# Kernel optimization log

Hardware: AMD Instinct MI355X
Metric: run time of the kernel (lower is better)

## Reference

```python
import jax, jax.numpy as jnp
import numpy as np

WS = 8          # window size
N = WS * WS     # tokens per window (64)
C = 256         # embed dim
H = 8           # heads
D = C // H      # head dim (32)
NW = 256        # windows per image
B_ = 2048       # total windows in batch (8 images * 256 windows)
CPB_HIDDEN = 512


def _make_relative_position_index():
    coords_h = np.arange(WS)
    coords_w = np.arange(WS)
    coords = np.stack(np.meshgrid(coords_h, coords_w, indexing='ij'))  # [2,WS,WS]
    coords = coords.reshape(2, -1)                                     # [2,N]
    rel = coords[:, :, None] - coords[:, None, :]                      # [2,N,N]
    rel = rel.transpose(1, 2, 0).astype(np.int64)                      # [N,N,2]
    rel[:, :, 0] += WS - 1
    rel[:, :, 1] += WS - 1
    rel[:, :, 0] *= 2 * WS - 1
    return rel.sum(-1)                                                 # [N,N]


def _make_relative_coords_table():
    rh = np.arange(-(WS - 1), WS, dtype=np.float64)
    rw = np.arange(-(WS - 1), WS, dtype=np.float64)
    tbl = np.stack(np.meshgrid(rh, rw, indexing='ij')).transpose(1, 2, 0)[None]  # [1,2W-1,2W-1,2]
    tbl[:, :, :, 0] /= (WS - 1)  # pretrained_window_size == window_size
    tbl[:, :, :, 1] /= (WS - 1)
    tbl *= 8
    tbl = np.sign(tbl) * np.log2(np.abs(tbl) + 1.0) / np.log2(8)
    return tbl.astype(np.float32)


def setup_inputs() -> dict:
    key = jax.random.key(0)
    ks = jax.random.split(key, 8)
    x = jax.random.normal(ks[0], (B_, N, C), dtype=jnp.float32)
    # shifted-window style additive mask: 0 for allowed, -100 for masked
    mask_bits = jax.random.uniform(ks[1], (NW, N, N)) < 0.1
    mask = jnp.where(mask_bits, jnp.float32(-100.0), jnp.float32(0.0))
    qkv_w = jax.random.normal(ks[2], (C, 3 * C), dtype=jnp.float32) * (1.0 / np.sqrt(C))
    q_bias = jnp.zeros((C,), jnp.float32)
    v_bias = jnp.zeros((C,), jnp.float32)
    logit_scale = jnp.full((H, 1, 1), np.log(10.0), dtype=jnp.float32)
    coords_table = jnp.asarray(_make_relative_coords_table())
    mlp1_w = jax.random.normal(ks[3], (2, CPB_HIDDEN), dtype=jnp.float32) * 0.5
    mlp1_b = jnp.zeros((CPB_HIDDEN,), jnp.float32)
    mlp2_w = jax.random.normal(ks[4], (CPB_HIDDEN, H), dtype=jnp.float32) * (1.0 / np.sqrt(CPB_HIDDEN))
    proj_w = jax.random.normal(ks[5], (C, C), dtype=jnp.float32) * (1.0 / np.sqrt(C))
    proj_b = jnp.zeros((C,), jnp.float32)
    rel_pos_index = jnp.asarray(_make_relative_position_index())  # [N,N] int64
    return {
        'x': x, 'mask': mask, 'qkv_w': qkv_w, 'q_bias': q_bias, 'v_bias': v_bias,
        'logit_scale': logit_scale, 'coords_table': coords_table,
        'mlp1_w': mlp1_w, 'mlp1_b': mlp1_b, 'mlp2_w': mlp2_w,
        'proj_w': proj_w, 'proj_b': proj_b, 'rel_pos_index': rel_pos_index,
    }


def _l2norm(t, axis=-1, eps=1e-12):
    n = jnp.sqrt(jnp.sum(t * t, axis=axis, keepdims=True))
    return t / jnp.maximum(n, eps)


def reference(x, mask, qkv_w, q_bias, v_bias, logit_scale, coords_table,
              mlp1_w, mlp1_b, mlp2_w, proj_w, proj_b, rel_pos_index):
    b, n, c = x.shape
    # qkv projection with (q_bias, 0, v_bias)
    qkv_bias = jnp.concatenate([q_bias, jnp.zeros_like(v_bias), v_bias], axis=0)
    qkv = x @ qkv_w + qkv_bias                          # [b, n, 3c]
    qkv = qkv.reshape(b, n, 3, H, D).transpose(2, 0, 3, 1, 4)  # [3, b, H, n, D]
    q, k, v = qkv[0], qkv[1], qkv[2]
    # cosine attention with learned per-head logit scale
    attn = jnp.einsum('bhnd,bhmd->bhnm', _l2norm(q), _l2norm(k))
    scale = jnp.exp(jnp.minimum(logit_scale, jnp.float32(np.log(1.0 / 0.01))))  # [H,1,1]
    attn = attn * scale[None]                           # [b, H, n, n]
    # continuous position bias MLP
    hbt = jax.nn.relu(coords_table @ mlp1_w + mlp1_b)   # [1, 2W-1, 2W-1, 512]
    bias_table = (hbt @ mlp2_w).reshape(-1, H)          # [(2W-1)^2, H]
    rel_bias = bias_table[rel_pos_index.reshape(-1)].reshape(n, n, H)
    rel_bias = 16.0 * jax.nn.sigmoid(rel_bias.transpose(2, 0, 1))  # [H, n, n]
    attn = attn + rel_bias[None]
    # shifted-window mask
    nw = mask.shape[0]
    attn = attn.reshape(b // nw, nw, H, n, n) + mask[None, :, None]
    attn = attn.reshape(b, H, n, n)
    attn = jax.nn.softmax(attn, axis=-1)
    out = jnp.einsum('bhnm,bhmd->bnhd', attn, v).reshape(b, n, c)
    return out @ proj_w + proj_b
```

## Files before the change

kernel.cpp:

```cpp
#include <hip/hip_runtime.h>
#include <hip/hip_bf16.h>
#include <stdint.h>

#define NTOK   64
#define CDIM   256
#define NHEAD  8
#define DHEAD  32
#define NWIN   256
#define BWIN   2048
#define MROWS  131072

typedef __attribute__((ext_vector_type(8))) short short8;
typedef __attribute__((ext_vector_type(4))) float f32x4;

__device__ __forceinline__ ushort f2bf(float f) {
  uint32_t u = __float_as_uint(f);
  u += 0x7fffu + ((u >> 16) & 1u);
  return (ushort)(u >> 16);
}
__device__ __forceinline__ void unpack8(uint4 u, float* f) {
  f[0] = __uint_as_float(u.x << 16);
  f[1] = __uint_as_float(u.x & 0xffff0000u);
  f[2] = __uint_as_float(u.y << 16);
  f[3] = __uint_as_float(u.y & 0xffff0000u);
  f[4] = __uint_as_float(u.z << 16);
  f[5] = __uint_as_float(u.z & 0xffff0000u);
  f[6] = __uint_as_float(u.w << 16);
  f[7] = __uint_as_float(u.w & 0xffff0000u);
}


__global__ void k_cast_bf16(const float* __restrict__ src, ushort* __restrict__ dst, int n4) {
  int i = blockIdx.x * blockDim.x + threadIdx.x;
  int stride = gridDim.x * blockDim.x;
  for (; i < n4; i += stride) {
    float4 v = ((const float4*)src)[i];
    ushort4 o;
    o.x = f2bf(v.x); o.y = f2bf(v.y); o.z = f2bf(v.z); o.w = f2bf(v.w);
    ((ushort4*)dst)[i] = o;
  }
}

__global__ void k_transpose_bf16(const float* __restrict__ src, ushort* __restrict__ dst, int K, int N) {
  int idx = blockIdx.x * 256 + threadIdx.x;
  if (idx < N * K) {
    int n = idx / K, k = idx - n * K;
    dst[idx] = f2bf(src[(size_t)k * N + n]);
  }
}

__global__ void k_cpb(const float* __restrict__ ct, const float* __restrict__ w1,
                      const float* __restrict__ b1, const float* __restrict__ w2,
                      float* __restrict__ out) {
  int p = blockIdx.x, t = threadIdx.x;
  float c0 = ct[p * 2], c1 = ct[p * 2 + 1];
  float acc[8];
#pragma unroll
  for (int h = 0; h < 8; ++h) acc[h] = 0.f;
  for (int j = t; j < 512; j += 256) {
    float hj = fmaxf(0.f, fmaf(c0, w1[j], fmaf(c1, w1[512 + j], b1[j])));
#pragma unroll
    for (int h = 0; h < 8; ++h) acc[h] = fmaf(hj, w2[j * 8 + h], acc[h]);
  }
#pragma unroll
  for (int off = 1; off < 64; off <<= 1)
#pragma unroll
    for (int h = 0; h < 8; ++h) acc[h] += __shfl_xor(acc[h], off, 64);
  __shared__ float red[4][8];
  if ((t & 63) == 0)
#pragma unroll
    for (int h = 0; h < 8; ++h) red[t >> 6][h] = acc[h];
  __syncthreads();
  if (t < 8) out[p * 8 + t] = red[0][t] + red[1][t] + red[2][t] + red[3][t];
}

__global__ void k_relbC(const float* __restrict__ bt, const int* __restrict__ rpi,
                        float* __restrict__ out) {
  int idx = blockIdx.x * 256 + threadIdx.x;
  int reg = idx & 3, l16 = (idx >> 2) & 15, g = (idx >> 6) & 3;
  int nt = (idx >> 8) & 3, mt = (idx >> 10) & 3, h = idx >> 12;
  int r = mt * 16 + g * 4 + reg, c = nt * 16 + l16;
  float v = bt[rpi[r * 64 + c] * 8 + h];
  out[idx] = 16.0f / (1.0f + __expf(-v));
}

__global__ void k_maskC(const float* __restrict__ mask, float* __restrict__ out) {
  int idx = blockIdx.x * 256 + threadIdx.x;
  int reg = idx & 3, l16 = (idx >> 2) & 15, g = (idx >> 6) & 3;
  int nt = (idx >> 8) & 3, mt = (idx >> 10) & 3, wi = idx >> 12;
  int r = mt * 16 + g * 4 + reg, c = nt * 16 + l16;
  out[idx] = mask[(size_t)wi * 4096 + r * 64 + c];
}

template <int MODE>
__global__ __launch_bounds__(256, 2) void gemm_bt(const ushort* __restrict__ A,
                                                  const ushort* __restrict__ BT,
                                                  void* __restrict__ Cout,
                                                  const float* __restrict__ bias0,
                                                  const float* __restrict__ bias1,
                                                  int K, int N) {
  __shared__ ushort As[128 * 64];
  __shared__ ushort Bs[128 * 64];
  const int t = threadIdx.x;
  const int bn = blockIdx.x, bm = blockIdx.y;
  const int wv = t >> 6, lane = t & 63, quad = lane >> 4, l16 = lane & 15;
  const int mbase = (wv & 1) * 64, nbase = (wv >> 1) * 64;

  f32x4 acc[4][4] = {};

  const int nkt = K >> 6;
  for (int kt = 0; kt < nkt; ++kt) {
    __syncthreads();
#pragma unroll
    for (int i = 0; i < 4; ++i) {
      int idx = i * 256 + t;
      int m = idx >> 3, c = idx & 7;
      int sw = (m * 8 + (c ^ (m & 7))) * 8;
      *(uint4*)(As + sw) = *(const uint4*)(A + (size_t)(bm * 128 + m) * K + kt * 64 + c * 8);
      *(uint4*)(Bs + sw) = *(const uint4*)(BT + (size_t)(bn * 128 + m) * K + kt * 64 + c * 8);
    }
    __syncthreads();
#pragma unroll
    for (int k2 = 0; k2 < 2; ++k2) {
      const int cidx = (k2 * 4 + quad) ^ (l16 & 7);
      short8 a[4], b[4];
#pragma unroll
      for (int mt = 0; mt < 4; ++mt)
        a[mt] = *(const short8*)(As + ((mbase + mt * 16 + l16) * 8 + cidx) * 8);
#pragma unroll
      for (int nt = 0; nt < 4; ++nt)
        b[nt] = *(const short8*)(Bs + ((nbase + nt * 16 + l16) * 8 + cidx) * 8);
#pragma unroll
      for (int mt = 0; mt < 4; ++mt)
#pragma unroll
        for (int nt = 0; nt < 4; ++nt)
          acc[mt][nt] = __builtin_amdgcn_mfma_f32_16x16x32_bf16(a[mt], b[nt], acc[mt][nt], 0, 0, 0);
    }
  }

#pragma unroll
  for (int mt = 0; mt < 4; ++mt)
#pragma unroll
    for (int nt = 0; nt < 4; ++nt) {
      int j = bn * 128 + nbase + nt * 16 + l16;
      int gm = bm * 128 + mbase + mt * 16 + quad * 4;
      float bs;
      if (MODE == 0) bs = (j < 256) ? bias0[j] : ((j < 512) ? 0.0f : bias1[j - 512]);
      else bs = bias0[j];
#pragma unroll
      for (int i2 = 0; i2 < 4; ++i2) {
        float v = acc[mt][nt][i2] + bs;
        size_t off = (size_t)(gm + i2) * N + j;
        if (MODE == 0) ((ushort*)Cout)[off] = f2bf(v);
        else ((float*)Cout)[off] = v;
      }
    }
}

__global__ __launch_bounds__(256, 2) void k_attn_mfma(const ushort* __restrict__ qkv,
                                                      const float* __restrict__ maskC,
                                                      const float* __restrict__ ls,
                                                      const float* __restrict__ relbC,
                                                      ushort* __restrict__ aob) {
  __shared__ ushort Qs[4][64][40];
  __shared__ ushort Ks[4][64][40];
  __shared__ ushort Vt[4][32][72];
  __shared__ ushort Ps[4][64][40];
  const int b = blockIdx.x, t = threadIdx.x;
  const int wi = b & (NWIN - 1);
  const int wv = t >> 6, lane = t & 63;
  const int g = lane >> 4, l16 = lane & 15;

  for (int pass = 0; pass < 2; ++pass) {
    __syncthreads();
    {
      const int hh = wv, tok = lane;
      const int h = pass * 4 + hh;
      const size_t base = ((size_t)b * 64 + tok) * 768 + h * 32;
      {
        union { uint4 u[4]; ushort s[32]; } raw, outp;
        raw.u[0] = *(const uint4*)(qkv + base);
        raw.u[1] = *(const uint4*)(qkv + base + 8);
        raw.u[2] = *(const uint4*)(qkv + base + 16);
        raw.u[3] = *(const uint4*)(qkv + base + 24);
        float f[32];
#pragma unroll
        for (int c = 0; c < 4; ++c) unpack8(raw.u[c], f + c * 8);
        float s = 0.f;
#pragma unroll
        for (int j = 0; j < 32; ++j) s = fmaf(f[j], f[j], s);
        float sc = __expf(fminf(ls[h], 4.6051701859880914f));
        float fac = sc / fmaxf(sqrtf(s), 1e-12f);
#pragma unroll
        for (int j = 0; j < 32; ++j) outp.s[j] = f2bf(f[j] * fac);
#pragma unroll
        for (int c = 0; c < 4; ++c) *(uint4*)&Qs[hh][tok][c * 8] = outp.u[c];
      }
      {
        union { uint4 u[4]; ushort s[32]; } raw, outp;
        raw.u[0] = *(const uint4*)(qkv + base + 256);
        raw.u[1] = *(const uint4*)(qkv + base + 264);
        raw.u[2] = *(const uint4*)(qkv + base + 272);
        raw.u[3] = *(const uint4*)(qkv + base + 280);
        float f[32];
#pragma unroll
        for (int c = 0; c < 4; ++c) unpack8(raw.u[c], f + c * 8);
        float s = 0.f;
#pragma unroll
        for (int j = 0; j < 32; ++j) s = fmaf(f[j], f[j], s);
        float fac = 1.0f / fmaxf(sqrtf(s), 1e-12f);
#pragma unroll
        for (int j = 0; j < 32; ++j) outp.s[j] = f2bf(f[j] * fac);
#pragma unroll
        for (int c = 0; c < 4; ++c) *(uint4*)&Ks[hh][tok][c * 8] = outp.u[c];
      }
      {
        union { uint4 u[4]; ushort s[32]; } raw;
        raw.u[0] = *(const uint4*)(qkv + base + 512);
        raw.u[1] = *(const uint4*)(qkv + base + 520);
        raw.u[2] = *(const uint4*)(qkv + base + 528);
        raw.u[3] = *(const uint4*)(qkv + base + 536);
#pragma unroll
        for (int d = 0; d < 32; ++d) Vt[hh][d][tok] = raw.s[d];
      }
    }
    __syncthreads();

    const int h = pass * 4 + wv;
    short8 qfr[4], kfr[4];
#pragma unroll
    for (int mt = 0; mt < 4; ++mt) qfr[mt] = *(const short8*)&Qs[wv][mt * 16 + l16][g * 8];
#pragma unroll
    for (int nt = 0; nt < 4; ++nt) kfr[nt] = *(const short8*)&Ks[wv][nt * 16 + l16][g * 8];
    f32x4 sv[4][4];
    const f32x4 zero = {0.f, 0.f, 0.f, 0.f};
#pragma unroll
    for (int mt = 0; mt < 4; ++mt)
#pragma unroll
      for (int nt = 0; nt < 4; ++nt)
        sv[mt][nt] = __builtin_amdgcn_mfma_f32_16x16x32_bf16(qfr[mt], kfr[nt], zero, 0, 0, 0);

#pragma unroll
    for (int mt = 0; mt < 4; ++mt)
#pragma unroll
      for (int nt = 0; nt < 4; ++nt) {
        float4 rb = *(const float4*)(relbC + (size_t)(((h * 4 + mt) * 4 + nt) * 4 + g) * 64 + l16 * 4);
        float4 mk = *(const float4*)(maskC + (size_t)(((wi * 4 + mt) * 4 + nt) * 4 + g) * 64 + l16 * 4);
        sv[mt][nt][0] += rb.x + mk.x;
        sv[mt][nt][1] += rb.y + mk.y;
        sv[mt][nt][2] += rb.z + mk.z;
        sv[mt][nt][3] += rb.w + mk.w;
      }

    float mx[4][4], inv[4][4];
#pragma unroll
    for (int mt = 0; mt < 4; ++mt)
#pragma unroll
      for (int reg = 0; reg < 4; ++reg) {
        float m = fmaxf(fmaxf(sv[mt][0][reg], sv[mt][1][reg]),
                        fmaxf(sv[mt][2][reg], sv[mt][3][reg]));
#pragma unroll
        for (int st = 1; st < 16; st <<= 1) m = fmaxf(m, __shfl_xor(m, st, 64));
        mx[mt][reg] = m;
      }
#pragma unroll
    for (int mt = 0; mt < 4; ++mt)
#pragma unroll
      for (int nt = 0; nt < 4; ++nt)
#pragma unroll
        for (int reg = 0; reg < 4; ++reg)
          sv[mt][nt][reg] = __expf(sv[mt][nt][reg] - mx[mt][reg]);
#pragma unroll
    for (int mt = 0; mt < 4; ++mt)
#pragma unroll
      for (int reg = 0; reg < 4; ++reg) {
        float s = sv[mt][0][reg] + sv[mt][1][reg] + sv[mt][2][reg] + sv[mt][3][reg];
#pragma unroll
        for (int st = 1; st < 16; st <<= 1) s += __shfl_xor(s, st, 64);
        inv[mt][reg] = 1.0f / s;
      }

    f32x4 ov[4][2] = {};
#pragma unroll
    for (int kt = 0; kt < 2; ++kt) {
      __syncthreads();
#pragma unroll
      for (int mt = 0; mt < 4; ++mt)
#pragma unroll
        for (int reg = 0; reg < 4; ++reg)
#pragma unroll
          for (int tjh = 0; tjh < 2; ++tjh)
            Ps[wv][mt * 16 + g * 4 + reg][tjh * 16 + l16] = f2bf(sv[mt][kt * 2 + tjh][reg]);
      __syncthreads();
      short8 pf[4], vf[2];
#pragma unroll
      for (int mt = 0; mt < 4; ++mt) pf[mt] = *(const short8*)&Ps[wv][mt * 16 + l16][g * 8];
#pragma unroll
      for (int n2 = 0; n2 < 2; ++n2) vf[n2] = *(const short8*)&Vt[wv][n2 * 16 + l16][kt * 32 + g * 8];
#pragma unroll
      for (int mt = 0; mt < 4; ++mt)
#pragma unroll
        for (int n2 = 0; n2 < 2; ++n2)
          ov[mt][n2] = __builtin_amdgcn_mfma_f32_16x16x32_bf16(pf[mt], vf[n2], ov[mt][n2], 0, 0, 0);
    }

#pragma unroll
    for (int mt = 0; mt < 4; ++mt)
#pragma unroll
      for (int n2 = 0; n2 < 2; ++n2)
#pragma unroll
        for (int reg = 0; reg < 4; ++reg) {
          int r = mt * 16 + g * 4 + reg;
          float o = ov[mt][n2][reg] * inv[mt][reg];
          aob[((size_t)b * 64 + r) * 256 + h * 32 + n2 * 16 + l16] = f2bf(o);
        }
  }
}


extern "C" void kernel_launch(void* const* d_in, const int* in_sizes, int n_in,
                              void* d_out, int out_size, void* d_ws, size_t ws_size,
                              hipStream_t stream) {
  const float* x      = (const float*)d_in[0];
  const float* mask   = (const float*)d_in[1];
  const float* qkv_w  = (const float*)d_in[2];
  const float* q_bias = (const float*)d_in[3];
  const float* v_bias = (const float*)d_in[4];
  const float* lscale = (const float*)d_in[5];
  const float* ctbl   = (const float*)d_in[6];
  const float* m1w    = (const float*)d_in[7];
  const float* m1b    = (const float*)d_in[8];
  const float* m2w    = (const float*)d_in[9];
  const float* projw  = (const float*)d_in[10];
  const float* projb  = (const float*)d_in[11];
  const int*   rpi    = (const int*)d_in[12];

  char* w = (char*)d_ws;
  float*  bias_table = (float*)(w + 0);
  float*  relbC      = (float*)(w + 8192);
  float*  maskC      = (float*)(w + 139264);
  ushort* qkvWT      = (ushort*)(w + 4333568);
  ushort* projWT     = (ushort*)(w + 4726784);
  ushort* xb         = (ushort*)(w + 4857856);
  ushort* qkvb       = (ushort*)(w + 71966720ull);
  ushort* aob        = (ushort*)(w + 273293312ull);
  (void)ws_size; (void)n_in; (void)in_sizes; (void)out_size;

  k_cast_bf16<<<4096, 256, 0, stream>>>(x, xb, MROWS * CDIM / 4);
  k_transpose_bf16<<<768, 256, 0, stream>>>(qkv_w, qkvWT, 256, 768);
  k_transpose_bf16<<<256, 256, 0, stream>>>(projw, projWT, 256, 256);
  k_cpb<<<225, 256, 0, stream>>>(ctbl, m1w, m1b, m2w, bias_table);
  k_relbC<<<128, 256, 0, stream>>>(bias_table, rpi, relbC);
  k_maskC<<<4096, 256, 0, stream>>>(mask, maskC);

  gemm_bt<0><<<dim3(6, 1024), 256, 0, stream>>>(xb, qkvWT, qkvb, q_bias, v_bias, 256, 768);
  k_attn_mfma<<<BWIN, 256, 0, stream>>>(qkvb, maskC, lscale, relbC, aob);
  gemm_bt<1><<<dim3(2, 1024), 256, 0, stream>>>(aob, projWT, d_out, projb, nullptr, 256, 256);
}
```

Baseline: 504.8 us.

## Load Q/K fragments straight into registers and drop block barriers in attention

Q and K are now read from global memory directly into the MFMA fragment layout, and the L2 norm is computed with cross-lane shuffles, so the Qs/Ks shared-memory staging is gone. Each wave only touches its own Vt and Ps slices, so every __syncthreads is removed and launch bounds move from 2 to 4 blocks per CU to raise occupancy. The softmax max, exp and sum loops are also merged. The costs are redundant, less coalesced global loads for Q/K and more register pressure under the tighter launch bound. Correctness now relies on each wave's own LDS writes being visible to its later reads without a barrier.

```diff
diff --git a/kernel.cpp b/kernel.cpp
--- a/kernel.cpp
+++ b/kernel.cpp
@@ -157,13 +157,11 @@
     }
 }
 
-__global__ __launch_bounds__(256, 2) void k_attn_mfma(const ushort* __restrict__ qkv,
+__global__ __launch_bounds__(256, 4) void k_attn_mfma(const ushort* __restrict__ qkv,
                                                       const float* __restrict__ maskC,
                                                       const float* __restrict__ ls,
                                                       const float* __restrict__ relbC,
                                                       ushort* __restrict__ aob) {
-  __shared__ ushort Qs[4][64][40];
-  __shared__ ushort Ks[4][64][40];
   __shared__ ushort Vt[4][32][72];
   __shared__ ushort Ps[4][64][40];
   const int b = blockIdx.x, t = threadIdx.x;
@@ -172,66 +170,53 @@
   const int g = lane >> 4, l16 = lane & 15;
 
   for (int pass = 0; pass < 2; ++pass) {
-    __syncthreads();
+    __builtin_amdgcn_s_waitcnt(0);
+    const int h = pass * 4 + wv;
+
     {
-      const int hh = wv, tok = lane;
-      const int h = pass * 4 + hh;
-      const size_t base = ((size_t)b * 64 + tok) * 768 + h * 32;
-      {
-        union { uint4 u[4]; ushort s[32]; } raw, outp;
-        raw.u[0] = *(const uint4*)(qkv + base);
-        raw.u[1] = *(const uint4*)(qkv + base + 8);
-        raw.u[2] = *(const uint4*)(qkv + base + 16);
-        raw.u[3] = *(const uint4*)(qkv + base + 24);
-        float f[32];
-#pragma unroll
-        for (int c = 0; c < 4; ++c) unpack8(raw.u[c], f + c * 8);
-        float s = 0.f;
-#pragma unroll
-        for (int j = 0; j < 32; ++j) s = fmaf(f[j], f[j], s);
-        float sc = __expf(fminf(ls[h], 4.6051701859880914f));
-        float fac = sc / fmaxf(sqrtf(s), 1e-12f);
-#pragma unroll
-        for (int j = 0; j < 32; ++j) outp.s[j] = f2bf(f[j] * fac);
-#pragma unroll
-        for (int c = 0; c < 4; ++c) *(uint4*)&Qs[hh][tok][c * 8] = outp.u[c];
-      }
-      {
-        union { uint4 u[4]; ushort s[32]; } raw, outp;
-        raw.u[0] = *(const uint4*)(qkv + base + 256);
-        raw.u[1] = *(const uint4*)(qkv + base + 264);
-        raw.u[2] = *(const uint4*)(qkv + base + 272);
-        raw.u[3] = *(const uint4*)(qkv + base + 280);
-        float f[32];
-#pragma unroll
-        for (int c = 0; c < 4; ++c) unpack8(raw.u[c], f + c * 8);
-        float s = 0.f;
-#pragma unroll
-        for (int j = 0; j < 32; ++j) s = fmaf(f[j], f[j], s);
-        float fac = 1.0f / fmaxf(sqrtf(s), 1e-12f);
-#pragma unroll
-        for (int j = 0; j < 32; ++j) outp.s[j] = f2bf(f[j] * fac);
-#pragma unroll
-        for (int c = 0; c < 4; ++c) *(uint4*)&Ks[hh][tok][c * 8] = outp.u[c];
-      }
-      {
-        union { uint4 u[4]; ushort s[32]; } raw;
-        raw.u[0] = *(const uint4*)(qkv + base + 512);
-        raw.u[1] = *(const uint4*)(qkv + base + 520);
-        raw.u[2] = *(const uint4*)(qkv + base + 528);
-        raw.u[3] = *(const uint4*)(qkv + base + 536);
-#pragma unroll
-        for (int d = 0; d < 32; ++d) Vt[hh][d][tok] = raw.s[d];
-      }
-    }
-    __syncthreads();
-
-    const int h = pass * 4 + wv;
+      const size_t base = ((size_t)b * 64 + lane) * 768 + 512 + h * 32;
+      union { uint4 u[4]; ushort s[32]; } raw;
+      raw.u[0] = *(const uint4*)(qkv + base);
+      raw.u[1] = *(const uint4*)(qkv + base + 8);
+      raw.u[2] = *(const uint4*)(qkv + base + 16);
+      raw.u[3] = *(const uint4*)(qkv + base + 24);
+#pragma unroll
+      for (int d = 0; d < 32; ++d) Vt[wv][d][lane] = raw.s[d];
+    }
+
+    const float lsc = __expf(fminf(ls[h], 4.6051701859880914f));
     short8 qfr[4], kfr[4];
 #pragma unroll
-    for (int mt = 0; mt < 4; ++mt) qfr[mt] = *(const short8*)&Qs[wv][mt * 16 + l16][g * 8];
-#pragma unroll
-    for (int nt = 0; nt < 4; ++nt) kfr[nt] = *(const short8*)&Ks[wv][nt * 16 + l16][g * 8];
+    for (int mt = 0; mt < 4; ++mt) {
+      size_t base = ((size_t)b * 64 + mt * 16 + l16) * 768 + h * 32 + g * 8;
+      uint4 raw = *(const uint4*)(qkv + base);
+      float f[8];
+      unpack8(raw, f);
+      float s = 0.f;
+#pragma unroll
+      for (int j = 0; j < 8; ++j) s = fmaf(f[j], f[j], s);
+      s += __shfl_xor(s, 16, 64);
+      s += __shfl_xor(s, 32, 64);
+      float fac = lsc / fmaxf(sqrtf(s), 1e-12f);
+#pragma unroll
+      for (int j = 0; j < 8; ++j) ((ushort*)&qfr[mt])[j] = f2bf(f[j] * fac);
+    }
+#pragma unroll
+    for (int nt = 0; nt < 4; ++nt) {
+      size_t base = ((size_t)b * 64 + nt * 16 + l16) * 768 + 256 + h * 32 + g * 8;
+      uint4 raw = *(const uint4*)(qkv + base);
+      float f[8];
+      unpack8(raw, f);
+      float s = 0.f;
+#pragma unroll
+      for (int j = 0; j < 8; ++j) s = fmaf(f[j], f[j], s);
+      s += __shfl_xor(s, 16, 64);
+      s += __shfl_xor(s, 32, 64);
+      float fac = 1.0f / fmaxf(sqrtf(s), 1e-12f);
+#pragma unroll
+      for (int j = 0; j < 8; ++j) ((ushort*)&kfr[nt])[j] = f2bf(f[j] * fac);
+    }
+
     f32x4 sv[4][4];
     const f32x4 zero = {0.f, 0.f, 0.f, 0.f};
 #pragma unroll
@@ -252,7 +237,7 @@
         sv[mt][nt][3] += rb.w + mk.w;
       }
 
-    float mx[4][4], inv[4][4];
+    float inv[4][4];
 #pragma unroll
     for (int mt = 0; mt < 4; ++mt)
 #pragma unroll
@@ -261,19 +246,9 @@
                         fmaxf(sv[mt][2][reg], sv[mt][3][reg]));
 #pragma unroll
         for (int st = 1; st < 16; st <<= 1) m = fmaxf(m, __shfl_xor(m, st, 64));
-        mx[mt][reg] = m;
-      }
-#pragma unroll
-    for (int mt = 0; mt < 4; ++mt)
-#pragma unroll
-      for (int nt = 0; nt < 4; ++nt)
-#pragma unroll
-        for (int reg = 0; reg < 4; ++reg)
-          sv[mt][nt][reg] = __expf(sv[mt][nt][reg] - mx[mt][reg]);
-#pragma unroll
-    for (int mt = 0; mt < 4; ++mt)
-#pragma unroll
-      for (int reg = 0; reg < 4; ++reg) {
+#pragma unroll
+        for (int nt = 0; nt < 4; ++nt)
+          sv[mt][nt][reg] = __expf(sv[mt][nt][reg] - m);
         float s = sv[mt][0][reg] + sv[mt][1][reg] + sv[mt][2][reg] + sv[mt][3][reg];
 #pragma unroll
         for (int st = 1; st < 16; st <<= 1) s += __shfl_xor(s, st, 64);
@@ -283,7 +258,6 @@
     f32x4 ov[4][2] = {};
 #pragma unroll
     for (int kt = 0; kt < 2; ++kt) {
-      __syncthreads();
 #pragma unroll
       for (int mt = 0; mt < 4; ++mt)
 #pragma unroll
@@ -291,7 +265,6 @@
 #pragma unroll
           for (int tjh = 0; tjh < 2; ++tjh)
             Ps[wv][mt * 16 + g * 4 + reg][tjh * 16 + l16] = f2bf(sv[mt][kt * 2 + tjh][reg]);
-      __syncthreads();
       short8 pf[4], vf[2];
 #pragma unroll
       for (int mt = 0; mt < 4; ++mt) pf[mt] = *(const short8*)&Ps[wv][mt * 16 + l16][g * 8];
```

New measurement: 611.8 us. 21.2% more time.
